# Optimization experiments

Hardware: AMD Instinct MI355X
Metric: run time of the kernel (lower is better)

The kernel has to match this reference:

```python
import jax, jax.numpy as jnp
import numpy as np

D_MODEL = 1024
NUM_HEADS = 16
HEAD_DIM = D_MODEL // NUM_HEADS  # 64
# NOTE: the torch module passes scale=attention_head_size (NOT 1/sqrt(dh));
# we reproduce that exact math: scores are MULTIPLIED by head_dim.
SCALE = float(HEAD_DIM)

B, S = 2, 2048


def setup_inputs() -> dict:
    key = jax.random.key(0)
    ks = jax.random.split(key, 6)
    q = jax.random.normal(ks[0], (B, S, D_MODEL), dtype=jnp.float32)
    k = jax.random.normal(ks[1], (B, S, D_MODEL), dtype=jnp.float32)
    v = jax.random.normal(ks[2], (B, S, D_MODEL), dtype=jnp.float32)
    # Linear weights stored as [in, out]; scaled like typical init so the
    # (head_dim-scaled) logits stay numerically sane.
    w_std = 0.02
    Wq = jax.random.normal(ks[3], (D_MODEL, D_MODEL), dtype=jnp.float32) * w_std
    Wk = jax.random.normal(ks[4], (D_MODEL, D_MODEL), dtype=jnp.float32) * w_std
    Wv = jax.random.normal(ks[5], (D_MODEL, D_MODEL), dtype=jnp.float32) * w_std
    return {"q": q, "k": k, "v": v, "Wq": Wq, "Wk": Wk, "Wv": Wv}


def reference(q, k, v, Wq, Wk, Wv):
    Bq, Sq, _ = q.shape
    # QKV projections (qkv_bias=False), split into heads: [B, S, H, dh]
    qh = (q @ Wq).reshape(Bq, Sq, NUM_HEADS, HEAD_DIM)
    kh = (k @ Wk).reshape(Bq, Sq, NUM_HEADS, HEAD_DIM)
    vh = (v @ Wv).reshape(Bq, Sq, NUM_HEADS, HEAD_DIM)
    # Full materialized scores [B, H, Sq, Sk] -- the naive MHA pattern.
    sims = jnp.einsum("bqhd,bkhd->bhqk", qh, kh) * SCALE
    attn = jax.nn.softmax(sims, axis=-1)
    # Second matmul, then merge heads back: [B, S, D]
    out = jnp.einsum("bhqk,bkhd->bqhd", attn, vh).reshape(Bq, Sq, D_MODEL)
    return out
```

## Files before the change

kernel.cpp:

```cpp
#include <hip/hip_runtime.h>
#include <cstdint>
#include <cstddef>

typedef unsigned short u16;
typedef __bf16 bf16x8 __attribute__((ext_vector_type(8)));
typedef float f32x4 __attribute__((ext_vector_type(4)));
typedef unsigned int u32x4 __attribute__((ext_vector_type(4)));
typedef unsigned int u32x2 __attribute__((ext_vector_type(2)));
typedef u16 u16x4 __attribute__((ext_vector_type(4)));

typedef __attribute__((address_space(3))) void lds_void;
typedef __attribute__((address_space(1))) void glb_void;

constexpr float CEXP = 92.33248261689366f;

constexpr size_t XSZ = 4096ull * 1024ull;
constexpr size_t WSZ = 1024ull * 1024ull;
constexpr size_t OFF_XQH = 0;
constexpr size_t OFF_XQL = OFF_XQH + XSZ;
constexpr size_t OFF_XKH = OFF_XQL + XSZ;
constexpr size_t OFF_XKL = OFF_XKH + XSZ;
constexpr size_t OFF_XVH = OFF_XKL + XSZ;
constexpr size_t OFF_XVL = OFF_XVH + XSZ;
constexpr size_t OFF_WQH = OFF_XVL + XSZ;
constexpr size_t OFF_WQL = OFF_WQH + WSZ;
constexpr size_t OFF_WKH = OFF_WQL + WSZ;
constexpr size_t OFF_WKL = OFF_WKH + WSZ;
constexpr size_t OFF_WVH = OFF_WKL + WSZ;
constexpr size_t OFF_WVL = OFF_WVH + WSZ;
constexpr size_t OFF_QH  = OFF_WVL + WSZ;
constexpr size_t OFF_QL  = OFF_QH + XSZ;
constexpr size_t OFF_KH  = OFF_QL + XSZ;
constexpr size_t OFF_KL  = OFF_KH + XSZ;
constexpr size_t OFF_VH  = OFF_KL + XSZ;
constexpr size_t OFF_VT  = OFF_VH + XSZ;

__device__ __forceinline__ u16 f2b(float f) {
  unsigned u = __builtin_bit_cast(unsigned, f);
  return (u16)((u + 0x7FFFu + ((u >> 16) & 1u)) >> 16);
}
__device__ __forceinline__ float b2f(u16 h) {
  return __builtin_bit_cast(float, ((unsigned)h) << 16);
}
__device__ __forceinline__ bf16x8 ld8(const u16* p) {
  return __builtin_bit_cast(bf16x8, *(const u32x4*)p);
}
__device__ __forceinline__ unsigned pk2(float a, float b) {
#if __has_builtin(__builtin_amdgcn_cvt_pk_bf16_f32)
  auto v = __builtin_amdgcn_cvt_pk_bf16_f32(a, b);
  return __builtin_bit_cast(unsigned, v);
#else
  return (unsigned)f2b(a) | ((unsigned)f2b(b) << 16);
#endif
}
__device__ __forceinline__ void glds16(const u16* g, u16* l) {
  __builtin_amdgcn_global_load_lds((const glb_void*)g, (lds_void*)l, 16, 0, 0);
}
__device__ __forceinline__ int swz32(int row, int cg) {
  return row * 32 + ((cg ^ ((row >> 1) & 3)) * 8);
}
__device__ __forceinline__ int swz64(int row, int cg) {
  return row * 64 + ((cg ^ (row & 7)) * 8);
}

__global__ __launch_bounds__(256) void convert_x3(const float* __restrict__ q,
                                                  const float* __restrict__ k,
                                                  const float* __restrict__ v,
                                                  u16* __restrict__ ws) {
  int z = blockIdx.y;
  const float* in = (z == 0) ? q : (z == 1) ? k : v;
  u16* hi = ws + ((z == 0) ? OFF_XQH : (z == 1) ? OFF_XKH : OFF_XVH);
  u16* lo = ws + ((z == 0) ? OFF_XQL : (z == 1) ? OFF_XKL : OFF_XVL);
  size_t i = ((size_t)blockIdx.x * 256u + threadIdx.x) * 4u;
  float4 vv = *(const float4*)(in + i);
  float a[4] = {vv.x, vv.y, vv.z, vv.w};
  u16x4 hv, lv;
#pragma unroll
  for (int j = 0; j < 4; ++j) {
    u16 hb = f2b(a[j]);
    hv[j] = hb;
    lv[j] = f2b(a[j] - b2f(hb));
  }
  *(u16x4*)(hi + i) = hv;
  *(u16x4*)(lo + i) = lv;
}

__global__ __launch_bounds__(256) void convert_w3(const float* __restrict__ Wq,
                                                  const float* __restrict__ Wk,
                                                  const float* __restrict__ Wv,
                                                  u16* __restrict__ ws) {
  int z = blockIdx.z;
  const float* W = (z == 0) ? Wq : (z == 1) ? Wk : Wv;
  u16* hiT = ws + ((z == 0) ? OFF_WQH : (z == 1) ? OFF_WKH : OFF_WVH);
  u16* loT = ws + ((z == 0) ? OFF_WQL : (z == 1) ? OFF_WKL : OFF_WVL);
  __shared__ float tile[32][33];
  int n0 = blockIdx.x * 32, k0 = blockIdx.y * 32;
  int t = threadIdx.x;
  int r = t >> 3, c0 = (t & 7) * 4;
  float4 v = *(const float4*)(W + (size_t)(k0 + r) * 1024 + n0 + c0);
  tile[r][c0] = v.x; tile[r][c0 + 1] = v.y; tile[r][c0 + 2] = v.z; tile[r][c0 + 3] = v.w;
  __syncthreads();
  u16x4 hv, lv;
#pragma unroll
  for (int j = 0; j < 4; ++j) {
    float x = tile[c0 + j][r];
    u16 hb = f2b(x);
    hv[j] = hb;
    lv[j] = f2b(x - b2f(hb));
  }
  size_t o = (size_t)(n0 + r) * 1024 + k0 + c0;
  *(u16x4*)(hiT + o) = hv;
  *(u16x4*)(loT + o) = lv;
}

__global__ __launch_bounds__(256) void gemm_qkv(u16* __restrict__ ws) {
  __shared__ u16 lah[128 * 32];
  __shared__ u16 lal[128 * 32];
  __shared__ u16 lbh[128 * 32];
  __shared__ u16 lbl[128 * 32];
  int z = blockIdx.z;
  const u16 *Ah, *Al, *Bh, *Bl; u16 *Oh, *Ol; bool split;
  if (z == 0)      { Ah = ws + OFF_XQH; Al = ws + OFF_XQL; Bh = ws + OFF_WQH; Bl = ws + OFF_WQL; Oh = ws + OFF_QH; Ol = ws + OFF_QL; split = true; }
  else if (z == 1) { Ah = ws + OFF_XKH; Al = ws + OFF_XKL; Bh = ws + OFF_WKH; Bl = ws + OFF_WKL; Oh = ws + OFF_KH; Ol = ws + OFF_KL; split = true; }
  else             { Ah = ws + OFF_XVH; Al = ws + OFF_XVH; Bh = ws + OFF_WVH; Bl = ws + OFF_WVH; Oh = ws + OFF_VH; Ol = nullptr;    split = false; }
  float oscale = (z == 0) ? CEXP : 1.0f;
  int m0 = blockIdx.y * 128, n0 = blockIdx.x * 128;
  int t = threadIdx.x, lane = t & 63, wave = t >> 6;
  int wm = (wave >> 1) * 64, wn = (wave & 1) * 64;
  int rl = lane >> 2, cgl = lane & 3;
  f32x4 acc[4][4] = {};
  for (int kb = 0; kb < 32; ++kb) {
    int k0 = kb * 32;
    __syncthreads();
#pragma unroll
    for (int i = 0; i < 2; ++i) {
      int row = wave * 32 + i * 16 + rl;
      int cgg = cgl ^ ((row >> 1) & 3);
      size_t ga = (size_t)(m0 + row) * 1024 + k0 + cgg * 8;
      size_t gb = (size_t)(n0 + row) * 1024 + k0 + cgg * 8;
      int lbase = (wave * 32 + i * 16) * 32;
      glds16(Ah + ga, &lah[lbase]);
      glds16(Bh + gb, &lbh[lbase]);
      if (split) {
        glds16(Al + ga, &lal[lbase]);
        glds16(Bl + gb, &lbl[lbase]);
      }
    }
    __syncthreads();
    int cg0 = lane >> 4;
    bf16x8 afh[4], afl[4], bfh[4], bfl[4];
#pragma unroll
    for (int i = 0; i < 4; ++i) {
      int ra = wm + i * 16 + (lane & 15);
      int rb = wn + i * 16 + (lane & 15);
      afh[i] = ld8(&lah[swz32(ra, cg0)]);
      bfh[i] = ld8(&lbh[swz32(rb, cg0)]);
      if (split) {
        afl[i] = ld8(&lal[swz32(ra, cg0)]);
        bfl[i] = ld8(&lbl[swz32(rb, cg0)]);
      }
    }
#pragma unroll
    for (int mt = 0; mt < 4; ++mt)
#pragma unroll
      for (int nt = 0; nt < 4; ++nt) {
        acc[mt][nt] = __builtin_amdgcn_mfma_f32_16x16x32_bf16(afh[mt], bfh[nt], acc[mt][nt], 0, 0, 0);
        if (split) {
          acc[mt][nt] = __builtin_amdgcn_mfma_f32_16x16x32_bf16(afl[mt], bfh[nt], acc[mt][nt], 0, 0, 0);
          acc[mt][nt] = __builtin_amdgcn_mfma_f32_16x16x32_bf16(afh[mt], bfl[nt], acc[mt][nt], 0, 0, 0);
        }
      }
  }
#pragma unroll
  for (int mt = 0; mt < 4; ++mt)
#pragma unroll
    for (int nt = 0; nt < 4; ++nt)
#pragma unroll
      for (int r = 0; r < 4; ++r) {
        int gm = m0 + wm + mt * 16 + (lane >> 4) * 4 + r;
        int gn = n0 + wn + nt * 16 + (lane & 15);
        int bb = gm >> 11, s = gm & 2047, hh = gn >> 6, d = gn & 63;
        size_t oi = ((size_t)(bb * 16 + hh) * 2048 + s) * 64 + d;
        float val = acc[mt][nt][r] * oscale;
        u16 hb = f2b(val);
        Oh[oi] = hb;
        if (Ol) Ol[oi] = f2b(val - b2f(hb));
      }
}

__global__ __launch_bounds__(256) void transpose_v(const u16* __restrict__ vh,
                                                   u16* __restrict__ vt) {
  __shared__ u16 tile[64][72];
  int bh = blockIdx.y;
  int s0 = blockIdx.x * 64;
  int t = threadIdx.x;
  for (int c = t; c < 512; c += 256) {
    int row = c >> 3, off = (c & 7) * 8;
    *(u32x4*)(&tile[row][off]) = *(const u32x4*)(vh + ((size_t)bh * 2048 + s0 + row) * 64 + off);
  }
  __syncthreads();
  int d = t >> 2, i0 = (t & 3) * 16;
  u16 vals[16];
#pragma unroll
  for (int i = 0; i < 16; ++i) vals[i] = tile[i0 + i][d];
  u16* outp = vt + ((size_t)bh * 64 + d) * 2048 + s0 + i0;
  *(u32x4*)(outp)     = *(u32x4*)(&vals[0]);
  *(u32x4*)(outp + 8) = *(u32x4*)(&vals[8]);
}

__global__ __launch_bounds__(256) void attn(const u16* __restrict__ ws,
                                            float* __restrict__ out) {
  __shared__ u16 lkh[64 * 64];
  __shared__ u16 lkl[64 * 64];
  __shared__ u16 lvt[64 * 64];
  __shared__ u16 lp[4][16 * 64];
  const u16* Qh = ws + OFF_QH; const u16* Ql = ws + OFF_QL;
  const u16* Kh = ws + OFF_KH; const u16* Kl = ws + OFF_KL;
  const u16* Vt = ws + OFF_VT;
  int b = blockIdx.z, h = blockIdx.y;
  int q0 = blockIdx.x * 64;
  int t = threadIdx.x, lane = t & 63, wave = t >> 6;
  int quad = lane >> 4, l15 = lane & 15;
  size_t hb = (size_t)(b * 16 + h) * (2048 * 64);
  bf16x8 onesf;
#pragma unroll
  for (int j = 0; j < 8; ++j) onesf[j] = __builtin_bit_cast(__bf16, (u16)0x3F80);
  int qrow = q0 + wave * 16 + l15;
  bf16x8 qfh[2], qfl[2];
#pragma unroll
  for (int ks = 0; ks < 2; ++ks) {
    size_t qo = hb + (size_t)qrow * 64 + ks * 32 + quad * 8;
    qfh[ks] = ld8(Qh + qo);
    qfl[ks] = ld8(Ql + qo);
  }
  float mi = -1e30f;
  f32x4 lsum = {};
  f32x4 o[4] = {};
  int rl = lane >> 3, cgl = lane & 7;

  for (int kt = 0; kt < 32; ++kt) {
    __syncthreads();
#pragma unroll
    for (int i = 0; i < 2; ++i) {
      int row = wave * 16 + i * 8 + rl;
      int cgg = cgl ^ (row & 7);
      int lbase = (wave * 16 + i * 8) * 64;
      size_t gk = hb + (size_t)(kt * 64 + row) * 64 + cgg * 8;
      glds16(Kh + gk, &lkh[lbase]);
      glds16(Kl + gk, &lkl[lbase]);
      size_t gv = hb + (size_t)row * 2048 + kt * 64 + cgg * 8;
      glds16(Vt + gv, &lvt[lbase]);
    }
    __syncthreads();
    f32x4 sc[4] = {};
#pragma unroll
    for (int nt = 0; nt < 4; ++nt) {
#pragma unroll
      for (int ks = 0; ks < 2; ++ks) {
        int so = swz64(nt * 16 + l15, ks * 4 + quad);
        bf16x8 kh_ = ld8(&lkh[so]);
        bf16x8 kl_ = ld8(&lkl[so]);
        sc[nt] = __builtin_amdgcn_mfma_f32_16x16x32_bf16(kh_, qfh[ks], sc[nt], 0, 0, 0);
        sc[nt] = __builtin_amdgcn_mfma_f32_16x16x32_bf16(kl_, qfh[ks], sc[nt], 0, 0, 0);
        sc[nt] = __builtin_amdgcn_mfma_f32_16x16x32_bf16(kh_, qfl[ks], sc[nt], 0, 0, 0);
      }
    }
    float mx = fmaxf(fmaxf(fmaxf(sc[0][0], sc[0][1]), fmaxf(sc[0][2], sc[0][3])),
                     fmaxf(fmaxf(sc[1][0], sc[1][1]), fmaxf(sc[1][2], sc[1][3])));
    float mx2 = fmaxf(fmaxf(fmaxf(sc[2][0], sc[2][1]), fmaxf(sc[2][2], sc[2][3])),
                      fmaxf(fmaxf(sc[3][0], sc[3][1]), fmaxf(sc[3][2], sc[3][3])));
    mx = fmaxf(mx, mx2);
    mx = fmaxf(mx, __shfl_xor(mx, 16));
    mx = fmaxf(mx, __shfl_xor(mx, 32));
    float mn = fmaxf(mi, mx);
    float alpha_s = exp2f(mi - mn);
    mi = mn;
    u16* lpw = &lp[wave][0];
    int r7 = l15 & 7;
#pragma unroll
    for (int nt = 0; nt < 4; ++nt) {
      float e0 = exp2f(sc[nt][0] - mn);
      float e1 = exp2f(sc[nt][1] - mn);
      float e2 = exp2f(sc[nt][2] - mn);
      float e3 = exp2f(sc[nt][3] - mn);
      unsigned u01 = pk2(e0, e1), u23 = pk2(e2, e3);
      int c = nt * 2 + (quad >> 1);
      int off = l15 * 64 + ((c ^ r7) * 8) + (quad & 1) * 4;
      *(u32x2*)(&lpw[off]) = u32x2{u01, u23};
    }
    float av[4];
#pragma unroll
    for (int r = 0; r < 4; ++r) av[r] = __shfl(alpha_s, quad * 4 + r);
#pragma unroll
    for (int r = 0; r < 4; ++r) {
      lsum[r] *= av[r];
      o[0][r] *= av[r]; o[1][r] *= av[r]; o[2][r] *= av[r]; o[3][r] *= av[r];
    }
    asm volatile("s_waitcnt lgkmcnt(0)" ::: "memory");
    bf16x8 pa[2];
#pragma unroll
    for (int ks = 0; ks < 2; ++ks)
      pa[ks] = ld8(&lpw[swz64(l15, ks * 4 + quad)]);
    lsum = __builtin_amdgcn_mfma_f32_16x16x32_bf16(pa[0], onesf, lsum, 0, 0, 0);
    lsum = __builtin_amdgcn_mfma_f32_16x16x32_bf16(pa[1], onesf, lsum, 0, 0, 0);
#pragma unroll
    for (int nt = 0; nt < 4; ++nt)
#pragma unroll
      for (int ks = 0; ks < 2; ++ks) {
        bf16x8 bv = ld8(&lvt[swz64(nt * 16 + l15, ks * 4 + quad)]);
        o[nt] = __builtin_amdgcn_mfma_f32_16x16x32_bf16(pa[ks], bv, o[nt], 0, 0, 0);
      }
  }
  float inv[4];
#pragma unroll
  for (int r = 0; r < 4; ++r) inv[r] = 1.0f / lsum[r];
#pragma unroll
  for (int nt = 0; nt < 4; ++nt)
#pragma unroll
    for (int r = 0; r < 4; ++r) {
      int srow = q0 + wave * 16 + quad * 4 + r;
      int d = nt * 16 + l15;
      out[(size_t)(b * 2048 + srow) * 1024 + h * 64 + d] = o[nt][r] * inv[r];
    }
}

extern "C" void kernel_launch(void* const* d_in, const int* in_sizes, int n_in,
                              void* d_out, int out_size, void* d_ws, size_t ws_size,
                              hipStream_t stream) {
  const float* q  = (const float*)d_in[0];
  const float* k  = (const float*)d_in[1];
  const float* v  = (const float*)d_in[2];
  const float* Wq = (const float*)d_in[3];
  const float* Wk = (const float*)d_in[4];
  const float* Wv = (const float*)d_in[5];
  u16* ws = (u16*)d_ws;
  float* out = (float*)d_out;

  convert_x3<<<dim3(4096, 3), 256, 0, stream>>>(q, k, v, ws);
  convert_w3<<<dim3(32, 32, 3), 256, 0, stream>>>(Wq, Wk, Wv, ws);
  gemm_qkv<<<dim3(8, 32, 3), 256, 0, stream>>>(ws);
  transpose_v<<<dim3(32, 32), 256, 0, stream>>>(ws + OFF_VH, ws + OFF_VT);
  attn<<<dim3(32, 16, 2), 256, 0, stream>>>(ws, out);
}
```

Baseline: 296.6 us.

## Fuse V transpose into QKV GEMM epilogue and double-buffer K/V tiles in attention

The V projection epilogue now writes its output directly in the transposed [b,h,d,s] layout with 4-wide packed stores, so the separate transpose_v kernel and its extra read/write pass over V go away. The attention kernel double-buffers its K-high, K-low and V^T LDS tiles, issuing the async global-to-LDS loads for the next tile before computing on the current one, with a single barrier per iteration. This is meant to hide global load latency behind the MFMA work. In exchange it doubles LDS use per block, which may lower occupancy, and the last iteration issues a redundant wraparound prefetch of tile 0.

```diff
diff --git a/kernel.cpp b/kernel.cpp
--- a/kernel.cpp
+++ b/kernel.cpp
@@ -32,8 +32,7 @@
 constexpr size_t OFF_QL  = OFF_QH + XSZ;
 constexpr size_t OFF_KH  = OFF_QL + XSZ;
 constexpr size_t OFF_KL  = OFF_KH + XSZ;
-constexpr size_t OFF_VH  = OFF_KL + XSZ;
-constexpr size_t OFF_VT  = OFF_VH + XSZ;
+constexpr size_t OFF_VT  = OFF_KL + XSZ;
 
 __device__ __forceinline__ u16 f2b(float f) {
   unsigned u = __builtin_bit_cast(unsigned, f);
@@ -122,7 +121,7 @@
   const u16 *Ah, *Al, *Bh, *Bl; u16 *Oh, *Ol; bool split;
   if (z == 0)      { Ah = ws + OFF_XQH; Al = ws + OFF_XQL; Bh = ws + OFF_WQH; Bl = ws + OFF_WQL; Oh = ws + OFF_QH; Ol = ws + OFF_QL; split = true; }
   else if (z == 1) { Ah = ws + OFF_XKH; Al = ws + OFF_XKL; Bh = ws + OFF_WKH; Bl = ws + OFF_WKL; Oh = ws + OFF_KH; Ol = ws + OFF_KL; split = true; }
-  else             { Ah = ws + OFF_XVH; Al = ws + OFF_XVH; Bh = ws + OFF_WVH; Bl = ws + OFF_WVH; Oh = ws + OFF_VH; Ol = nullptr;    split = false; }
+  else             { Ah = ws + OFF_XVH; Al = ws + OFF_XVH; Bh = ws + OFF_WVH; Bl = ws + OFF_WVH; Oh = ws + OFF_VT; Ol = nullptr;    split = false; }
   float oscale = (z == 0) ? CEXP : 1.0f;
   int m0 = blockIdx.y * 128, n0 = blockIdx.x * 128;
   int t = threadIdx.x, lane = t & 63, wave = t >> 6;
@@ -171,48 +170,43 @@
         }
       }
   }
-#pragma unroll
-  for (int mt = 0; mt < 4; ++mt)
-#pragma unroll
-    for (int nt = 0; nt < 4; ++nt)
-#pragma unroll
-      for (int r = 0; r < 4; ++r) {
-        int gm = m0 + wm + mt * 16 + (lane >> 4) * 4 + r;
+  if (z == 2) {
+#pragma unroll
+    for (int mt = 0; mt < 4; ++mt)
+#pragma unroll
+      for (int nt = 0; nt < 4; ++nt) {
+        int s_base = m0 + wm + mt * 16 + (lane >> 4) * 4;
         int gn = n0 + wn + nt * 16 + (lane & 15);
-        int bb = gm >> 11, s = gm & 2047, hh = gn >> 6, d = gn & 63;
-        size_t oi = ((size_t)(bb * 16 + hh) * 2048 + s) * 64 + d;
-        float val = acc[mt][nt][r] * oscale;
-        u16 hb = f2b(val);
-        Oh[oi] = hb;
-        if (Ol) Ol[oi] = f2b(val - b2f(hb));
-      }
-}
-
-__global__ __launch_bounds__(256) void transpose_v(const u16* __restrict__ vh,
-                                                   u16* __restrict__ vt) {
-  __shared__ u16 tile[64][72];
-  int bh = blockIdx.y;
-  int s0 = blockIdx.x * 64;
-  int t = threadIdx.x;
-  for (int c = t; c < 512; c += 256) {
-    int row = c >> 3, off = (c & 7) * 8;
-    *(u32x4*)(&tile[row][off]) = *(const u32x4*)(vh + ((size_t)bh * 2048 + s0 + row) * 64 + off);
-  }
-  __syncthreads();
-  int d = t >> 2, i0 = (t & 3) * 16;
-  u16 vals[16];
-#pragma unroll
-  for (int i = 0; i < 16; ++i) vals[i] = tile[i0 + i][d];
-  u16* outp = vt + ((size_t)bh * 64 + d) * 2048 + s0 + i0;
-  *(u32x4*)(outp)     = *(u32x4*)(&vals[0]);
-  *(u32x4*)(outp + 8) = *(u32x4*)(&vals[8]);
+        int bb = s_base >> 11, s = s_base & 2047, hh = gn >> 6, d = gn & 63;
+        u16x4 hv;
+#pragma unroll
+        for (int r = 0; r < 4; ++r) hv[r] = f2b(acc[mt][nt][r]);
+        *(u16x4*)(Oh + ((size_t)((bb * 16 + hh) * 64 + d)) * 2048 + s) = hv;
+      }
+  } else {
+#pragma unroll
+    for (int mt = 0; mt < 4; ++mt)
+#pragma unroll
+      for (int nt = 0; nt < 4; ++nt)
+#pragma unroll
+        for (int r = 0; r < 4; ++r) {
+          int gm = m0 + wm + mt * 16 + (lane >> 4) * 4 + r;
+          int gn = n0 + wn + nt * 16 + (lane & 15);
+          int bb = gm >> 11, s = gm & 2047, hh = gn >> 6, d = gn & 63;
+          size_t oi = ((size_t)(bb * 16 + hh) * 2048 + s) * 64 + d;
+          float val = acc[mt][nt][r] * oscale;
+          u16 hb = f2b(val);
+          Oh[oi] = hb;
+          Ol[oi] = f2b(val - b2f(hb));
+        }
+  }
 }
 
 __global__ __launch_bounds__(256) void attn(const u16* __restrict__ ws,
                                             float* __restrict__ out) {
-  __shared__ u16 lkh[64 * 64];
-  __shared__ u16 lkl[64 * 64];
-  __shared__ u16 lvt[64 * 64];
+  __shared__ u16 lkh[2][64 * 64];
+  __shared__ u16 lkl[2][64 * 64];
+  __shared__ u16 lvt[2][64 * 64];
   __shared__ u16 lp[4][16 * 64];
   const u16* Qh = ws + OFF_QH; const u16* Ql = ws + OFF_QL;
   const u16* Kh = ws + OFF_KH; const u16* Kl = ws + OFF_KL;
@@ -238,28 +232,34 @@
   f32x4 o[4] = {};
   int rl = lane >> 3, cgl = lane & 7;
 
-  for (int kt = 0; kt < 32; ++kt) {
-    __syncthreads();
+  auto stage = [&](int kt, int bsel) {
 #pragma unroll
     for (int i = 0; i < 2; ++i) {
       int row = wave * 16 + i * 8 + rl;
       int cgg = cgl ^ (row & 7);
       int lbase = (wave * 16 + i * 8) * 64;
       size_t gk = hb + (size_t)(kt * 64 + row) * 64 + cgg * 8;
-      glds16(Kh + gk, &lkh[lbase]);
-      glds16(Kl + gk, &lkl[lbase]);
+      glds16(Kh + gk, &lkh[bsel][lbase]);
+      glds16(Kl + gk, &lkl[bsel][lbase]);
       size_t gv = hb + (size_t)row * 2048 + kt * 64 + cgg * 8;
-      glds16(Vt + gv, &lvt[lbase]);
-    }
-    __syncthreads();
+      glds16(Vt + gv, &lvt[bsel][lbase]);
+    }
+  };
+
+  stage(0, 0);
+  __syncthreads();
+
+  for (int kt = 0; kt < 32; ++kt) {
+    int cur = kt & 1;
+    stage((kt + 1) & 31, cur ^ 1);
     f32x4 sc[4] = {};
 #pragma unroll
     for (int nt = 0; nt < 4; ++nt) {
 #pragma unroll
       for (int ks = 0; ks < 2; ++ks) {
         int so = swz64(nt * 16 + l15, ks * 4 + quad);
-        bf16x8 kh_ = ld8(&lkh[so]);
-        bf16x8 kl_ = ld8(&lkl[so]);
+        bf16x8 kh_ = ld8(&lkh[cur][so]);
+        bf16x8 kl_ = ld8(&lkl[cur][so]);
         sc[nt] = __builtin_amdgcn_mfma_f32_16x16x32_bf16(kh_, qfh[ks], sc[nt], 0, 0, 0);
         sc[nt] = __builtin_amdgcn_mfma_f32_16x16x32_bf16(kl_, qfh[ks], sc[nt], 0, 0, 0);
         sc[nt] = __builtin_amdgcn_mfma_f32_16x16x32_bf16(kh_, qfl[ks], sc[nt], 0, 0, 0);
@@ -307,9 +307,10 @@
     for (int nt = 0; nt < 4; ++nt)
 #pragma unroll
       for (int ks = 0; ks < 2; ++ks) {
-        bf16x8 bv = ld8(&lvt[swz64(nt * 16 + l15, ks * 4 + quad)]);
+        bf16x8 bv = ld8(&lvt[cur][swz64(nt * 16 + l15, ks * 4 + quad)]);
         o[nt] = __builtin_amdgcn_mfma_f32_16x16x32_bf16(pa[ks], bv, o[nt], 0, 0, 0);
       }
+    __syncthreads();
   }
   float inv[4];
 #pragma unroll
@@ -339,6 +340,5 @@
   convert_x3<<<dim3(4096, 3), 256, 0, stream>>>(q, k, v, ws);
   convert_w3<<<dim3(32, 32, 3), 256, 0, stream>>>(Wq, Wk, Wv, ws);
   gemm_qkv<<<dim3(8, 32, 3), 256, 0, stream>>>(ws);
-  transpose_v<<<dim3(32, 32), 256, 0, stream>>>(ws + OFF_VH, ws + OFF_VT);
   attn<<<dim3(32, 16, 2), 256, 0, stream>>>(ws, out);
 }
```

New measurement: 312.9 us. +5.5%, slower.

## Stage QKV GEMM epilogue through LDS and remap blocks for XCD locality

Applied to the files above, without the earlier changes.

The GEMM epilogue now writes bf16 results into a swizzled shared-memory tile and then stores full 128-byte head rows with 16-byte vector stores, replacing scattered 2-byte global stores. The launch becomes a 1D grid whose block index is remapped so that the 8 N-tiles sharing an M row panel (and the same weight matrix) land on the same XCD, aiming for better L2 reuse. The change adds extra barriers and a second LDS round for the low-part output.

```diff
diff --git a/kernel.cpp b/kernel.cpp
--- a/kernel.cpp
+++ b/kernel.cpp
@@ -114,17 +114,24 @@
 }
 
 __global__ __launch_bounds__(256) void gemm_qkv(u16* __restrict__ ws) {
-  __shared__ u16 lah[128 * 32];
-  __shared__ u16 lal[128 * 32];
-  __shared__ u16 lbh[128 * 32];
-  __shared__ u16 lbl[128 * 32];
-  int z = blockIdx.z;
+  __shared__ u16 smem[4][128 * 32];
+  u16* lah = smem[0]; u16* lal = smem[1];
+  u16* lbh = smem[2]; u16* lbl = smem[3];
+  u16* cbuf = &smem[0][0];
+
+  int id = blockIdx.x;
+  int xcd = id & 7, seq = id >> 3;
+  int pair = xcd * 12 + (seq >> 3);
+  int tile_n = seq & 7;
+  int z = pair >> 5;
+  int tile_m = pair & 31;
+
   const u16 *Ah, *Al, *Bh, *Bl; u16 *Oh, *Ol; bool split;
   if (z == 0)      { Ah = ws + OFF_XQH; Al = ws + OFF_XQL; Bh = ws + OFF_WQH; Bl = ws + OFF_WQL; Oh = ws + OFF_QH; Ol = ws + OFF_QL; split = true; }
   else if (z == 1) { Ah = ws + OFF_XKH; Al = ws + OFF_XKL; Bh = ws + OFF_WKH; Bl = ws + OFF_WKL; Oh = ws + OFF_KH; Ol = ws + OFF_KL; split = true; }
   else             { Ah = ws + OFF_XVH; Al = ws + OFF_XVH; Bh = ws + OFF_WVH; Bl = ws + OFF_WVH; Oh = ws + OFF_VH; Ol = nullptr;    split = false; }
   float oscale = (z == 0) ? CEXP : 1.0f;
-  int m0 = blockIdx.y * 128, n0 = blockIdx.x * 128;
+  int m0 = tile_m * 128, n0 = tile_n * 128;
   int t = threadIdx.x, lane = t & 63, wave = t >> 6;
   int wm = (wave >> 1) * 64, wn = (wave & 1) * 64;
   int rl = lane >> 2, cgl = lane & 3;
@@ -171,21 +178,37 @@
         }
       }
   }
-#pragma unroll
-  for (int mt = 0; mt < 4; ++mt)
-#pragma unroll
-    for (int nt = 0; nt < 4; ++nt)
-#pragma unroll
-      for (int r = 0; r < 4; ++r) {
-        int gm = m0 + wm + mt * 16 + (lane >> 4) * 4 + r;
-        int gn = n0 + wn + nt * 16 + (lane & 15);
-        int bb = gm >> 11, s = gm & 2047, hh = gn >> 6, d = gn & 63;
-        size_t oi = ((size_t)(bb * 16 + hh) * 2048 + s) * 64 + d;
-        float val = acc[mt][nt][r] * oscale;
-        u16 hb = f2b(val);
-        Oh[oi] = hb;
-        if (Ol) Ol[oi] = f2b(val - b2f(hb));
-      }
+  auto epi_round = [&](u16* dst, bool lo_round) {
+#pragma unroll
+    for (int mt = 0; mt < 4; ++mt)
+#pragma unroll
+      for (int nt = 0; nt < 4; ++nt)
+#pragma unroll
+        for (int r = 0; r < 4; ++r) {
+          int row = wm + mt * 16 + (lane >> 4) * 4 + r;
+          int col = wn + nt * 16 + (lane & 15);
+          float v = acc[mt][nt][r] * oscale;
+          u16 hb = f2b(v);
+          u16 val = lo_round ? f2b(v - b2f(hb)) : hb;
+          cbuf[row * 128 + (((col >> 3) ^ (row & 15)) * 8) + (col & 7)] = val;
+        }
+    __syncthreads();
+    int orow = t >> 1, half = t & 1;
+    int gm = m0 + orow, bb = gm >> 11, s = gm & 2047;
+    int hh = (n0 >> 6) + half;
+    u16* gp = dst + ((size_t)(bb * 16 + hh) * 2048 + s) * 64;
+#pragma unroll
+    for (int i = 0; i < 8; ++i) {
+      int phys = (half * 8 + i) ^ (orow & 15);
+      *(u32x4*)(gp + i * 8) = *(const u32x4*)(&cbuf[orow * 128 + phys * 8]);
+    }
+  };
+  __syncthreads();
+  epi_round(Oh, false);
+  if (Ol) {
+    __syncthreads();
+    epi_round(Ol, true);
+  }
 }
 
 __global__ __launch_bounds__(256) void transpose_v(const u16* __restrict__ vh,
@@ -338,7 +361,7 @@
 
   convert_x3<<<dim3(4096, 3), 256, 0, stream>>>(q, k, v, ws);
   convert_w3<<<dim3(32, 32, 3), 256, 0, stream>>>(Wq, Wk, Wv, ws);
-  gemm_qkv<<<dim3(8, 32, 3), 256, 0, stream>>>(ws);
+  gemm_qkv<<<768, 256, 0, stream>>>(ws);
   transpose_v<<<dim3(32, 32), 256, 0, stream>>>(ws + OFF_VH, ws + OFF_VT);
   attn<<<dim3(32, 16, 2), 256, 0, stream>>>(ws, out);
 }
```

After: 348.4 us. 17.5% more time.
